# Kernel optimization log

Measured on AMD Instinct MI355X. Metric: run time of the kernel, lower is better.

The kernel has to match this reference:

```python
import jax, jax.numpy as jnp
import numpy as np

T, B, I, H = 2000, 32, 320, 320
SLOPE = 0.2  # hard_sigmoid_slope


def _hard_sigmoid(x):
    return jnp.clip(SLOPE * x + 0.5, 0.0, 1.0)


def setup_inputs() -> dict:
    key = jax.random.key(0)
    ks = jax.random.split(key, 5)
    stdv = 1.0 / np.sqrt(H)
    u = lambda k, s: jax.random.uniform(k, s, jnp.float32, -stdv, stdv)
    return {
        "x": jax.random.normal(ks[0], (T, B, I), jnp.float32),
        "weight_ih": u(ks[1], (4 * H, I)),
        "weight_hh": u(ks[2], (4 * H, H)),
        "bias_ih": u(ks[3], (4 * H,)),
        "bias_hh": u(ks[4], (4 * H,)),
    }


def reference(x, weight_ih, weight_hh, bias_ih, bias_hh):
    # Precompute input-side gate projection for all timesteps (one big GEMM):
    # gates_x[t] = x[t] @ W_ih^T + b_ih + b_hh   -> [T, B, 4H]
    gates_x = jnp.einsum("tbi,gi->tbg", x, weight_ih) + bias_ih + bias_hh

    h0 = jnp.zeros((x.shape[1], weight_hh.shape[1]), x.dtype)
    c0 = jnp.zeros_like(h0)

    def step(carry, gx_t):
        h, c = carry
        gates = gx_t + h @ weight_hh.T  # [B, 4H]
        i, f, g, o = jnp.split(gates, 4, axis=-1)
        i = _hard_sigmoid(i)
        f = _hard_sigmoid(f)
        g = jnp.clip(g, -1.0, 1.0)  # hardtanh
        o = _hard_sigmoid(o)
        c1 = f * c + i * g  # delta is None -> no clamp of c1
        h1 = o * jnp.clip(c1, -1.0, 1.0)
        return (h1, c1), h1

    (_, _), out = jax.lax.scan(step, (h0, c0), gates_x)
    return out  # [T, B, H]
```

## Files before the change

kernel.cpp:

```cpp
#include <hip/hip_runtime.h>
#include <stdint.h>


#define T_STEPS 2000
#define BATCH   32
#define IDIM    320
#define HDIM    320
#define NWG     20
#define WPG     10
#define NTH     512
#define GB      16
#define UPW     32
#define LDK     328
#define HSLOT   (BATCH*HDIM)

typedef __attribute__((ext_vector_type(8))) short short8;
typedef __attribute__((ext_vector_type(4))) float f32x4;
typedef __attribute__((ext_vector_type(4))) unsigned short ushort4v;
typedef __attribute__((ext_vector_type(4))) unsigned int uint32x4;

static __device__ __forceinline__ unsigned short f2bf(float f) {
    uint32_t u = __float_as_uint(f);
    u += 0x7FFFu + ((u >> 16) & 1u);
    return (unsigned short)(u >> 16);
}
static __device__ __forceinline__ float bf2f(unsigned short s) {
    return __uint_as_float(((uint32_t)s) << 16);
}
static __device__ __forceinline__ float sat01(float v)  { return fminf(fmaxf(v, 0.f), 1.f); }
static __device__ __forceinline__ float clamp1(float v) { return fminf(fmaxf(v, -1.f), 1.f); }

static __device__ __forceinline__ void cvt_store(unsigned short* hi_p,
                                                 unsigned short* lo_p, float4 v) {
    ushort4v hi, lo;
    hi[0] = f2bf(v.x); lo[0] = f2bf(v.x - bf2f(hi[0]));
    hi[1] = f2bf(v.y); lo[1] = f2bf(v.y - bf2f(hi[1]));
    hi[2] = f2bf(v.z); lo[2] = f2bf(v.z - bf2f(hi[2]));
    hi[3] = f2bf(v.w); lo[3] = f2bf(v.w - bf2f(hi[3]));
    *(ushort4v*)hi_p = hi;
    *(ushort4v*)lo_p = lo;
}

__global__ __launch_bounds__(NTH, 2)
void hard_lstm(const float* __restrict__ x, const float* __restrict__ w_ih,
               const float* __restrict__ w_hh, const float* __restrict__ b_ih,
               const float* __restrict__ b_hh, float* __restrict__ out,
               unsigned short* __restrict__ hb, uint32_t* __restrict__ flags)
{
    __shared__ __align__(16) unsigned short xb[2][2][GB][LDK];
    __shared__ __align__(16) unsigned short h1s[2][GB][UPW];

    const int tid  = threadIdx.x;
    const int wgg  = blockIdx.x;
    const int grp  = wgg / WPG;
    const int wgl  = wgg % WPG;
    const int wave = tid >> 6;
    const int lane = tid & 63;
    const int col  = lane & 15;
    const int q    = lane >> 4;

    short8 ahi[20], alo[20];
    {
        const int jA   = wgl * UPW + wave * 4 + (col >> 2);
        const int grow = (col & 3) * HDIM + jA;
        const float* wi = w_ih + (size_t)grow * IDIM;
        const float* wh = w_hh + (size_t)grow * HDIM;
        #pragma unroll
        for (int s = 0; s < 20; ++s) {
            #pragma unroll
            for (int jj = 0; jj < 8; ++jj) {
                int k = s * 32 + q * 8 + jj;
                float w = (k < IDIM) ? wi[k] : wh[k - IDIM];
                unsigned short hi = f2bf(w);
                ahi[s][jj] = (short)hi;
                alo[s][jj] = (short)f2bf(w - bf2f(hi));
            }
        }
    }

    const int jOut = wgl * UPW + wave * 4 + q;
    const int bOut = grp * GB + col;
    float bias4[4];
    #pragma unroll
    for (int v = 0; v < 4; ++v)
        bias4[v] = b_ih[v * HDIM + jOut] + b_hh[v * HDIM + jOut];

    const int i0 = tid, i1 = tid + NTH, i2 = tid + 2 * NTH;
    const int sb0 = i0 / 80, sk0 = (i0 % 80) * 4;
    const int sb1 = i1 / 80, sk1 = (i1 % 80) * 4;
    const int sb2 = i2 / 80, sk2 = (i2 % 80) * 4;
    const bool has2 = (i2 < 1280);

    uint32_t* fline = flags + grp * 16;
    uint32_t* fpoll = &fline[lane % WPG];

    const unsigned short* hp0 = hb + (size_t)bOut * HDIM + q * 8;

    h1s[1][col][wave * 4 + q] = 0;
    {
        const float4* xs = (const float4*)(x + (size_t)(grp * GB) * IDIM);
        float4 v0 = xs[i0], v1 = xs[i1], v2 = {};
        if (has2) v2 = xs[i2];
        cvt_store(&xb[0][0][sb0][sk0], &xb[0][1][sb0][sk0], v0);
        cvt_store(&xb[0][0][sb1][sk1], &xb[0][1][sb1][sk1], v1);
        if (has2) cvt_store(&xb[0][0][sb2][sk2], &xb[0][1][sb2][sk2], v2);
    }
    __syncthreads();
    if (wave == 0) {
        const int b = lane >> 2, part = lane & 3;
        uint32x4 d = *(const uint32x4*)&h1s[1][b][part * 8];
        unsigned short* dst = hb + (size_t)(grp * GB + b) * HDIM + wgl * UPW + part * 8;
        asm volatile("global_store_dwordx4 %0, %1, off sc0 sc1\n\t"
                     "s_waitcnt vmcnt(0)" :: "v"(dst), "v"(d) : "memory");
        if (lane == 0)
            __hip_atomic_store(&fline[wgl], 1u, __ATOMIC_RELAXED, __HIP_MEMORY_SCOPE_SYSTEM);
    }

    float c_state = 0.f;

    #pragma unroll 1
    for (int t = 0; t < T_STEPS; ++t) {
        const int slot  = t & 1;
        const int slotn = slot ^ 1;

        float4 xr0 = {}, xr1 = {}, xr2 = {};
        const bool havex = (t + 1 < T_STEPS);
        if (havex) {
            const float4* xs = (const float4*)(x + ((size_t)(t + 1) * BATCH + grp * GB) * IDIM);
            xr0 = xs[i0]; xr1 = xs[i1];
            if (has2) xr2 = xs[i2];
        }

        {
            const uint32_t tgt = (uint32_t)(t + 1);
            while (true) {
                uint32_t v = __hip_atomic_load(fpoll, __ATOMIC_RELAXED,
                                               __HIP_MEMORY_SCOPE_SYSTEM);
                if (__all((int)(v >= tgt))) break;
            }
        }

        uint32x4 hv[10];
        {
            const unsigned short* hp = hp0 + (size_t)slot * HSLOT;
            asm volatile(
                "global_load_dwordx4 %0, %10, off sc0 sc1\n\t"
                "global_load_dwordx4 %1, %10, off offset:64 sc0 sc1\n\t"
                "global_load_dwordx4 %2, %10, off offset:128 sc0 sc1\n\t"
                "global_load_dwordx4 %3, %10, off offset:192 sc0 sc1\n\t"
                "global_load_dwordx4 %4, %10, off offset:256 sc0 sc1\n\t"
                "global_load_dwordx4 %5, %10, off offset:320 sc0 sc1\n\t"
                "global_load_dwordx4 %6, %10, off offset:384 sc0 sc1\n\t"
                "global_load_dwordx4 %7, %10, off offset:448 sc0 sc1\n\t"
                "global_load_dwordx4 %8, %10, off offset:512 sc0 sc1\n\t"
                "global_load_dwordx4 %9, %10, off offset:576 sc0 sc1\n\t"
                "s_waitcnt vmcnt(0)"
                : "=&v"(hv[0]), "=&v"(hv[1]), "=&v"(hv[2]), "=&v"(hv[3]), "=&v"(hv[4]),
                  "=&v"(hv[5]), "=&v"(hv[6]), "=&v"(hv[7]), "=&v"(hv[8]), "=&v"(hv[9])
                : "v"(hp) : "memory");
        }

        f32x4 acc0 = {0.f, 0.f, 0.f, 0.f};
        f32x4 acc1 = {0.f, 0.f, 0.f, 0.f};
        f32x4 acc2 = {0.f, 0.f, 0.f, 0.f};
        {
            const unsigned short* bxh = &xb[slot][0][col][q * 8];
            const unsigned short* bxl = &xb[slot][1][col][q * 8];
            #pragma unroll
            for (int s = 0; s < 10; ++s) {
                short8 bh = *(const short8*)(bxh + s * 32);
                short8 bl = *(const short8*)(bxl + s * 32);
                acc0 = __builtin_amdgcn_mfma_f32_16x16x32_bf16(ahi[s], bh, acc0, 0, 0, 0);
                acc1 = __builtin_amdgcn_mfma_f32_16x16x32_bf16(alo[s], bh, acc1, 0, 0, 0);
                acc2 = __builtin_amdgcn_mfma_f32_16x16x32_bf16(ahi[s], bl, acc2, 0, 0, 0);
            }
            #pragma unroll
            for (int s = 0; s < 10; ++s) {
                short8 bh = *(const short8*)&hv[s];
                acc0 = __builtin_amdgcn_mfma_f32_16x16x32_bf16(ahi[10 + s], bh, acc0, 0, 0, 0);
                acc1 = __builtin_amdgcn_mfma_f32_16x16x32_bf16(alo[10 + s], bh, acc1, 0, 0, 0);
            }
        }

        float p[4];
        #pragma unroll
        for (int v = 0; v < 4; ++v) p[v] = acc0[v] + acc1[v] + acc2[v] + bias4[v];
        float gi = sat01(0.2f * p[0] + 0.5f);
        float gf = sat01(0.2f * p[1] + 0.5f);
        float gg = clamp1(p[2]);
        float go = sat01(0.2f * p[3] + 0.5f);
        c_state = gf * c_state + gi * gg;
        float h1 = go * clamp1(c_state);

        h1s[slot][col][wave * 4 + q] = f2bf(h1);

        if (havex) {
            cvt_store(&xb[slotn][0][sb0][sk0], &xb[slotn][1][sb0][sk0], xr0);
            cvt_store(&xb[slotn][0][sb1][sk1], &xb[slotn][1][sb1][sk1], xr1);
            if (has2) cvt_store(&xb[slotn][0][sb2][sk2], &xb[slotn][1][sb2][sk2], xr2);
        }

        out[(size_t)t * (BATCH * HDIM) + (size_t)bOut * HDIM + jOut] = h1;

        __syncthreads();

        if (wave == 0) {
            const int b = lane >> 2, part = lane & 3;
            uint32x4 d = *(const uint32x4*)&h1s[slot][b][part * 8];
            unsigned short* dst = hb + (size_t)slotn * HSLOT
                                + (size_t)(grp * GB + b) * HDIM + wgl * UPW + part * 8;
            asm volatile("global_store_dwordx4 %0, %1, off sc0 sc1\n\t"
                         "s_waitcnt vmcnt(0)" :: "v"(dst), "v"(d) : "memory");
            if (lane == 0)
                __hip_atomic_store(&fline[wgl], (uint32_t)(t + 2), __ATOMIC_RELAXED,
                                   __HIP_MEMORY_SCOPE_SYSTEM);
        }
    }
}

extern "C" void kernel_launch(void* const* d_in, const int* in_sizes, int n_in,
                              void* d_out, int out_size, void* d_ws, size_t ws_size,
                              hipStream_t stream) {
    const float* x   = (const float*)d_in[0];
    const float* wih = (const float*)d_in[1];
    const float* whh = (const float*)d_in[2];
    const float* bih = (const float*)d_in[3];
    const float* bhh = (const float*)d_in[4];
    float* out = (float*)d_out;

    unsigned short* hb = (unsigned short*)d_ws;
    uint32_t* flags = (uint32_t*)((char*)d_ws + (size_t)2 * HSLOT * 2);

    hipMemsetAsync(flags, 0, 2 * 16 * sizeof(uint32_t), stream);

    void* args[] = {(void*)&x, (void*)&wih, (void*)&whh, (void*)&bih, (void*)&bhh,
                    (void*)&out, (void*)&hb, (void*)&flags};
    hipError_t e = hipLaunchCooperativeKernel((const void*)hard_lstm, dim3(NWG), dim3(NTH),
                                              args, 0, stream);
    if (e != hipSuccess) {
        hipLaunchKernelGGL(hard_lstm, dim3(NWG), dim3(NTH), 0, stream,
                           x, wih, whh, bih, bhh, out, hb, flags);
    }
}
```

Baseline: 9.267 ms.

## Pack step tag with hidden value to replace flag-based inter-workgroup sync

Each thread now writes its bf16 hidden value packed with a 16-bit timestep tag into a 32-bit word in global memory. Consumers poll the data words themselves until every tag matches, so a separate flag store and its wait-for-completion are no longer needed. The received values are staged into LDS for the MFMA B operand, which adds a block barrier before the recurrent GEMM. The old end-of-step barrier and single-wave publish are removed. This halves the density of hidden data, spins on a larger polled footprint, and relies on the 16-bit tag wrap staying unambiguous.

```diff
diff --git a/kernel.cpp b/kernel.cpp
--- a/kernel.cpp
+++ b/kernel.cpp
@@ -11,8 +11,9 @@
 #define NTH     512
 #define GB      16
 #define UPW     32
-#define LDK     328
-#define HSLOT   (BATCH*HDIM)
+#define LDK     324
+#define GSZ     (GB*HDIM)
+#define SSZ     (BATCH*HDIM)
 
 typedef __attribute__((ext_vector_type(8))) short short8;
 typedef __attribute__((ext_vector_type(4))) float f32x4;
@@ -29,6 +30,10 @@
 }
 static __device__ __forceinline__ float sat01(float v)  { return fminf(fmaxf(v, 0.f), 1.f); }
 static __device__ __forceinline__ float clamp1(float v) { return fminf(fmaxf(v, -1.f), 1.f); }
+
+static __device__ __forceinline__ void st_dword_l3(uint32_t* p, uint32_t v) {
+    asm volatile("global_store_dword %0, %1, off sc0 sc1" :: "v"(p), "v"(v) : "memory");
+}
 
 static __device__ __forceinline__ void cvt_store(unsigned short* hi_p,
                                                  unsigned short* lo_p, float4 v) {
@@ -45,10 +50,10 @@
 void hard_lstm(const float* __restrict__ x, const float* __restrict__ w_ih,
                const float* __restrict__ w_hh, const float* __restrict__ b_ih,
                const float* __restrict__ b_hh, float* __restrict__ out,
-               unsigned short* __restrict__ hb, uint32_t* __restrict__ flags)
+               uint32_t* __restrict__ hb32)
 {
     __shared__ __align__(16) unsigned short xb[2][2][GB][LDK];
-    __shared__ __align__(16) unsigned short h1s[2][GB][UPW];
+    __shared__ __align__(16) unsigned short hbl[2][GB][LDK];
 
     const int tid  = threadIdx.x;
     const int wgg  = blockIdx.x;
@@ -85,35 +90,23 @@
     for (int v = 0; v < 4; ++v)
         bias4[v] = b_ih[v * HDIM + jOut] + b_hh[v * HDIM + jOut];
 
-    const int i0 = tid, i1 = tid + NTH, i2 = tid + 2 * NTH;
-    const int sb0 = i0 / 80, sk0 = (i0 % 80) * 4;
-    const int sb1 = i1 / 80, sk1 = (i1 % 80) * 4;
-    const int sb2 = i2 / 80, sk2 = (i2 % 80) * 4;
-    const bool has2 = (i2 < 1280);
-
-    uint32_t* fline = flags + grp * 16;
-    uint32_t* fpoll = &fline[lane % WPG];
-
-    const unsigned short* hp0 = hb + (size_t)bOut * HDIM + q * 8;
-
-    h1s[1][col][wave * 4 + q] = 0;
+    const int c0 = tid, c1 = tid + NTH, c2 = tid + 2 * NTH;
+    const int b0 = c0 / 80, k0 = (c0 % 80) * 4;
+    const int b1 = c1 / 80, k1 = (c1 % 80) * 4;
+    const int b2 = c2 / 80, k2 = (c2 % 80) * 4;
+    const bool has2 = (tid < 256);
+
+    uint32_t* hSelf0 = hb32 + grp * GSZ + col * HDIM + jOut;
+    const uint32_t* hPollBase = hb32 + grp * GSZ;
+
+    st_dword_l3(hSelf0, 1u);
     {
         const float4* xs = (const float4*)(x + (size_t)(grp * GB) * IDIM);
-        float4 v0 = xs[i0], v1 = xs[i1], v2 = {};
-        if (has2) v2 = xs[i2];
-        cvt_store(&xb[0][0][sb0][sk0], &xb[0][1][sb0][sk0], v0);
-        cvt_store(&xb[0][0][sb1][sk1], &xb[0][1][sb1][sk1], v1);
-        if (has2) cvt_store(&xb[0][0][sb2][sk2], &xb[0][1][sb2][sk2], v2);
-    }
-    __syncthreads();
-    if (wave == 0) {
-        const int b = lane >> 2, part = lane & 3;
-        uint32x4 d = *(const uint32x4*)&h1s[1][b][part * 8];
-        unsigned short* dst = hb + (size_t)(grp * GB + b) * HDIM + wgl * UPW + part * 8;
-        asm volatile("global_store_dwordx4 %0, %1, off sc0 sc1\n\t"
-                     "s_waitcnt vmcnt(0)" :: "v"(dst), "v"(d) : "memory");
-        if (lane == 0)
-            __hip_atomic_store(&fline[wgl], 1u, __ATOMIC_RELAXED, __HIP_MEMORY_SCOPE_SYSTEM);
+        float4 v0 = xs[c0], v1 = xs[c1], v2 = {};
+        if (has2) v2 = xs[c2];
+        cvt_store(&xb[0][0][b0][k0], &xb[0][1][b0][k0], v0);
+        cvt_store(&xb[0][0][b1][k1], &xb[0][1][b1][k1], v1);
+        if (has2) cvt_store(&xb[0][0][b2][k2], &xb[0][1][b2][k2], v2);
     }
 
     float c_state = 0.f;
@@ -127,38 +120,49 @@
         const bool havex = (t + 1 < T_STEPS);
         if (havex) {
             const float4* xs = (const float4*)(x + ((size_t)(t + 1) * BATCH + grp * GB) * IDIM);
-            xr0 = xs[i0]; xr1 = xs[i1];
-            if (has2) xr2 = xs[i2];
-        }
-
+            xr0 = xs[c0]; xr1 = xs[c1];
+            if (has2) xr2 = xs[c2];
+        }
+
+        uint32x4 a0, a1, a2;
         {
             const uint32_t tgt = (uint32_t)(t + 1);
-            while (true) {
-                uint32_t v = __hip_atomic_load(fpoll, __ATOMIC_RELAXED,
-                                               __HIP_MEMORY_SCOPE_SYSTEM);
-                if (__all((int)(v >= tgt))) break;
-            }
-        }
-
-        uint32x4 hv[10];
+            const uint32_t* pb = hPollBase + (size_t)slot * SSZ;
+            const uint32_t* p0 = pb + c0 * 4;
+            const uint32_t* p1 = pb + c1 * 4;
+            const uint32_t* p2 = pb + (has2 ? c2 * 4 : c0 * 4);
+            uint32_t mm;
+            do {
+                asm volatile(
+                    "global_load_dwordx4 %0, %3, off sc0 sc1\n\t"
+                    "global_load_dwordx4 %1, %4, off sc0 sc1\n\t"
+                    "global_load_dwordx4 %2, %5, off sc0 sc1\n\t"
+                    "s_waitcnt vmcnt(0)"
+                    : "=&v"(a0), "=&v"(a1), "=&v"(a2)
+                    : "v"(p0), "v"(p1), "v"(p2)
+                    : "memory");
+                mm = (a0[0] ^ tgt) | (a0[1] ^ tgt) | (a0[2] ^ tgt) | (a0[3] ^ tgt)
+                   | (a1[0] ^ tgt) | (a1[1] ^ tgt) | (a1[2] ^ tgt) | (a1[3] ^ tgt);
+                if (has2)
+                    mm |= (a2[0] ^ tgt) | (a2[1] ^ tgt) | (a2[2] ^ tgt) | (a2[3] ^ tgt);
+            } while (mm & 0xffffu);
+        }
+
         {
-            const unsigned short* hp = hp0 + (size_t)slot * HSLOT;
-            asm volatile(
-                "global_load_dwordx4 %0, %10, off sc0 sc1\n\t"
-                "global_load_dwordx4 %1, %10, off offset:64 sc0 sc1\n\t"
-                "global_load_dwordx4 %2, %10, off offset:128 sc0 sc1\n\t"
-                "global_load_dwordx4 %3, %10, off offset:192 sc0 sc1\n\t"
-                "global_load_dwordx4 %4, %10, off offset:256 sc0 sc1\n\t"
-                "global_load_dwordx4 %5, %10, off offset:320 sc0 sc1\n\t"
-                "global_load_dwordx4 %6, %10, off offset:384 sc0 sc1\n\t"
-                "global_load_dwordx4 %7, %10, off offset:448 sc0 sc1\n\t"
-                "global_load_dwordx4 %8, %10, off offset:512 sc0 sc1\n\t"
-                "global_load_dwordx4 %9, %10, off offset:576 sc0 sc1\n\t"
-                "s_waitcnt vmcnt(0)"
-                : "=&v"(hv[0]), "=&v"(hv[1]), "=&v"(hv[2]), "=&v"(hv[3]), "=&v"(hv[4]),
-                  "=&v"(hv[5]), "=&v"(hv[6]), "=&v"(hv[7]), "=&v"(hv[8]), "=&v"(hv[9])
-                : "v"(hp) : "memory");
-        }
+            ushort4v v0 = {(unsigned short)(a0[0] >> 16), (unsigned short)(a0[1] >> 16),
+                           (unsigned short)(a0[2] >> 16), (unsigned short)(a0[3] >> 16)};
+            ushort4v v1 = {(unsigned short)(a1[0] >> 16), (unsigned short)(a1[1] >> 16),
+                           (unsigned short)(a1[2] >> 16), (unsigned short)(a1[3] >> 16)};
+            *(ushort4v*)&hbl[slot][b0][k0] = v0;
+            *(ushort4v*)&hbl[slot][b1][k1] = v1;
+            if (has2) {
+                ushort4v v2 = {(unsigned short)(a2[0] >> 16), (unsigned short)(a2[1] >> 16),
+                               (unsigned short)(a2[2] >> 16), (unsigned short)(a2[3] >> 16)};
+                *(ushort4v*)&hbl[slot][b2][k2] = v2;
+            }
+        }
+
+        __syncthreads();
 
         f32x4 acc0 = {0.f, 0.f, 0.f, 0.f};
         f32x4 acc1 = {0.f, 0.f, 0.f, 0.f};
@@ -166,6 +170,7 @@
         {
             const unsigned short* bxh = &xb[slot][0][col][q * 8];
             const unsigned short* bxl = &xb[slot][1][col][q * 8];
+            const unsigned short* bhp = &hbl[slot][col][q * 8];
             #pragma unroll
             for (int s = 0; s < 10; ++s) {
                 short8 bh = *(const short8*)(bxh + s * 32);
@@ -176,7 +181,7 @@
             }
             #pragma unroll
             for (int s = 0; s < 10; ++s) {
-                short8 bh = *(const short8*)&hv[s];
+                short8 bh = *(const short8*)(bhp + s * 32);
                 acc0 = __builtin_amdgcn_mfma_f32_16x16x32_bf16(ahi[10 + s], bh, acc0, 0, 0, 0);
                 acc1 = __builtin_amdgcn_mfma_f32_16x16x32_bf16(alo[10 + s], bh, acc1, 0, 0, 0);
             }
@@ -192,28 +197,15 @@
         c_state = gf * c_state + gi * gg;
         float h1 = go * clamp1(c_state);
 
-        h1s[slot][col][wave * 4 + q] = f2bf(h1);
+        uint32_t dpk = ((uint32_t)f2bf(h1) << 16) | ((uint32_t)(t + 2) & 0xffffu);
+        st_dword_l3(hSelf0 + (size_t)slotn * SSZ, dpk);
+
+        out[(size_t)t * SSZ + (size_t)bOut * HDIM + jOut] = h1;
 
         if (havex) {
-            cvt_store(&xb[slotn][0][sb0][sk0], &xb[slotn][1][sb0][sk0], xr0);
-            cvt_store(&xb[slotn][0][sb1][sk1], &xb[slotn][1][sb1][sk1], xr1);
-            if (has2) cvt_store(&xb[slotn][0][sb2][sk2], &xb[slotn][1][sb2][sk2], xr2);
-        }
-
-        out[(size_t)t * (BATCH * HDIM) + (size_t)bOut * HDIM + jOut] = h1;
-
-        __syncthreads();
-
-        if (wave == 0) {
-            const int b = lane >> 2, part = lane & 3;
-            uint32x4 d = *(const uint32x4*)&h1s[slot][b][part * 8];
-            unsigned short* dst = hb + (size_t)slotn * HSLOT
-                                + (size_t)(grp * GB + b) * HDIM + wgl * UPW + part * 8;
-            asm volatile("global_store_dwordx4 %0, %1, off sc0 sc1\n\t"
-                         "s_waitcnt vmcnt(0)" :: "v"(dst), "v"(d) : "memory");
-            if (lane == 0)
-                __hip_atomic_store(&fline[wgl], (uint32_t)(t + 2), __ATOMIC_RELAXED,
-                                   __HIP_MEMORY_SCOPE_SYSTEM);
+            cvt_store(&xb[slotn][0][b0][k0], &xb[slotn][1][b0][k0], xr0);
+            cvt_store(&xb[slotn][0][b1][k1], &xb[slotn][1][b1][k1], xr1);
+            if (has2) cvt_store(&xb[slotn][0][b2][k2], &xb[slotn][1][b2][k2], xr2);
         }
     }
 }
@@ -228,17 +220,16 @@
     const float* bhh = (const float*)d_in[4];
     float* out = (float*)d_out;
 
-    unsigned short* hb = (unsigned short*)d_ws;
-    uint32_t* flags = (uint32_t*)((char*)d_ws + (size_t)2 * HSLOT * 2);
-
-    hipMemsetAsync(flags, 0, 2 * 16 * sizeof(uint32_t), stream);
+    uint32_t* hb32 = (uint32_t*)d_ws;
+
+    hipMemsetAsync(hb32, 0, (size_t)2 * SSZ * 4, stream);
 
     void* args[] = {(void*)&x, (void*)&wih, (void*)&whh, (void*)&bih, (void*)&bhh,
-                    (void*)&out, (void*)&hb, (void*)&flags};
+                    (void*)&out, (void*)&hb32};
     hipError_t e = hipLaunchCooperativeKernel((const void*)hard_lstm, dim3(NWG), dim3(NTH),
                                               args, 0, stream);
     if (e != hipSuccess) {
         hipLaunchKernelGGL(hard_lstm, dim3(NWG), dim3(NTH), 0, stream,
-                           x, wih, whh, bih, bhh, out, hb, flags);
-    }
-}
+                           x, wih, whh, bih, bhh, out, hb32);
+    }
+}
```

Result: slower. 16.03 ms (+73.0%).

## Poll flags with wave 0 only and move x staging off the critical path

Applied to the files above, without the earlier changes.

Only wave 0 now spins on the cross-workgroup flags, at agent scope instead of system scope, and a block barrier then releases the other waves. The x prefetch and its bf16 conversion move after the h publish and are done only by waves 1-7, so wave 0 can store h and raise its flag sooner. The LDS row stride changes from 328 to 324. The aim is to shorten the per-step serial chain between workgroups, at the cost of one extra barrier per step and a different LDS bank pattern.

```diff
diff --git a/kernel.cpp b/kernel.cpp
--- a/kernel.cpp
+++ b/kernel.cpp
@@ -11,8 +11,8 @@
 #define NTH     512
 #define GB      16
 #define UPW     32
-#define LDK     328
-#define HSLOT   (BATCH*HDIM)
+#define LDK     324
+#define SSZ     (BATCH*HDIM)
 
 typedef __attribute__((ext_vector_type(8))) short short8;
 typedef __attribute__((ext_vector_type(4))) float f32x4;
@@ -85,11 +85,13 @@
     for (int v = 0; v < 4; ++v)
         bias4[v] = b_ih[v * HDIM + jOut] + b_hh[v * HDIM + jOut];
 
-    const int i0 = tid, i1 = tid + NTH, i2 = tid + 2 * NTH;
-    const int sb0 = i0 / 80, sk0 = (i0 % 80) * 4;
-    const int sb1 = i1 / 80, sk1 = (i1 % 80) * 4;
-    const int sb2 = i2 / 80, sk2 = (i2 % 80) * 4;
-    const bool has2 = (i2 < 1280);
+    const bool stg  = (tid >= 64);
+    const int  sidx = stg ? (tid - 64) : 0;
+    const int  c0 = sidx, c1 = sidx + 448, c2 = (sidx < 384) ? sidx + 896 : sidx;
+    const bool has2 = stg && (sidx < 384);
+    const int  b0 = c0 / 80, k0 = (c0 % 80) * 4;
+    const int  b1 = c1 / 80, k1 = (c1 % 80) * 4;
+    const int  b2 = c2 / 80, k2 = (c2 % 80) * 4;
 
     uint32_t* fline = flags + grp * 16;
     uint32_t* fpoll = &fline[lane % WPG];
@@ -97,13 +99,13 @@
     const unsigned short* hp0 = hb + (size_t)bOut * HDIM + q * 8;
 
     h1s[1][col][wave * 4 + q] = 0;
-    {
+    if (stg) {
         const float4* xs = (const float4*)(x + (size_t)(grp * GB) * IDIM);
-        float4 v0 = xs[i0], v1 = xs[i1], v2 = {};
-        if (has2) v2 = xs[i2];
-        cvt_store(&xb[0][0][sb0][sk0], &xb[0][1][sb0][sk0], v0);
-        cvt_store(&xb[0][0][sb1][sk1], &xb[0][1][sb1][sk1], v1);
-        if (has2) cvt_store(&xb[0][0][sb2][sk2], &xb[0][1][sb2][sk2], v2);
+        float4 v0 = xs[c0], v1 = xs[c1], v2 = {};
+        if (has2) v2 = xs[c2];
+        cvt_store(&xb[0][0][b0][k0], &xb[0][1][b0][k0], v0);
+        cvt_store(&xb[0][0][b1][k1], &xb[0][1][b1][k1], v1);
+        if (has2) cvt_store(&xb[0][0][b2][k2], &xb[0][1][b2][k2], v2);
     }
     __syncthreads();
     if (wave == 0) {
@@ -123,26 +125,19 @@
         const int slot  = t & 1;
         const int slotn = slot ^ 1;
 
-        float4 xr0 = {}, xr1 = {}, xr2 = {};
-        const bool havex = (t + 1 < T_STEPS);
-        if (havex) {
-            const float4* xs = (const float4*)(x + ((size_t)(t + 1) * BATCH + grp * GB) * IDIM);
-            xr0 = xs[i0]; xr1 = xs[i1];
-            if (has2) xr2 = xs[i2];
-        }
-
-        {
+        if (wave == 0) {
             const uint32_t tgt = (uint32_t)(t + 1);
             while (true) {
                 uint32_t v = __hip_atomic_load(fpoll, __ATOMIC_RELAXED,
-                                               __HIP_MEMORY_SCOPE_SYSTEM);
+                                               __HIP_MEMORY_SCOPE_AGENT);
                 if (__all((int)(v >= tgt))) break;
             }
         }
+        __syncthreads();
 
         uint32x4 hv[10];
         {
-            const unsigned short* hp = hp0 + (size_t)slot * HSLOT;
+            const unsigned short* hp = hp0 + (size_t)slot * SSZ;
             asm volatile(
                 "global_load_dwordx4 %0, %10, off sc0 sc1\n\t"
                 "global_load_dwordx4 %1, %10, off offset:64 sc0 sc1\n\t"
@@ -194,26 +189,28 @@
 
         h1s[slot][col][wave * 4 + q] = f2bf(h1);
 
-        if (havex) {
-            cvt_store(&xb[slotn][0][sb0][sk0], &xb[slotn][1][sb0][sk0], xr0);
-            cvt_store(&xb[slotn][0][sb1][sk1], &xb[slotn][1][sb1][sk1], xr1);
-            if (has2) cvt_store(&xb[slotn][0][sb2][sk2], &xb[slotn][1][sb2][sk2], xr2);
-        }
-
-        out[(size_t)t * (BATCH * HDIM) + (size_t)bOut * HDIM + jOut] = h1;
-
         __syncthreads();
 
         if (wave == 0) {
             const int b = lane >> 2, part = lane & 3;
             uint32x4 d = *(const uint32x4*)&h1s[slot][b][part * 8];
-            unsigned short* dst = hb + (size_t)slotn * HSLOT
+            unsigned short* dst = hb + (size_t)slotn * SSZ
                                 + (size_t)(grp * GB + b) * HDIM + wgl * UPW + part * 8;
             asm volatile("global_store_dwordx4 %0, %1, off sc0 sc1\n\t"
                          "s_waitcnt vmcnt(0)" :: "v"(dst), "v"(d) : "memory");
             if (lane == 0)
                 __hip_atomic_store(&fline[wgl], (uint32_t)(t + 2), __ATOMIC_RELAXED,
                                    __HIP_MEMORY_SCOPE_SYSTEM);
+        }
+
+        out[(size_t)t * SSZ + (size_t)bOut * HDIM + jOut] = h1;
+        if (stg && (t + 1 < T_STEPS)) {
+            const float4* xs = (const float4*)(x + ((size_t)(t + 1) * BATCH + grp * GB) * IDIM);
+            float4 v0 = xs[c0], v1 = xs[c1], v2 = {};
+            if (has2) v2 = xs[c2];
+            cvt_store(&xb[slotn][0][b0][k0], &xb[slotn][1][b0][k0], v0);
+            cvt_store(&xb[slotn][0][b1][k1], &xb[slotn][1][b1][k1], v1);
+            if (has2) cvt_store(&xb[slotn][0][b2][k2], &xb[slotn][1][b2][k2], v2);
         }
     }
 }
@@ -229,7 +226,7 @@
     float* out = (float*)d_out;
 
     unsigned short* hb = (unsigned short*)d_ws;
-    uint32_t* flags = (uint32_t*)((char*)d_ws + (size_t)2 * HSLOT * 2);
+    uint32_t* flags = (uint32_t*)((char*)d_ws + (size_t)2 * SSZ * 2);
 
     hipMemsetAsync(flags, 0, 2 * 16 * sizeof(uint32_t), stream);
 
```

Result: slower. 14.07 ms (+51.8%).
